# Optimization experiments

Hardware: AMD Instinct MI355X
Metric: run time of the kernel (lower is better)

Reference implementation:

```python
import jax, jax.numpy as jnp
import numpy as np

B, T, D, E, H = 4, 2048, 1024, 8, 1024  # H = hidden_units // num_experts


def setup_inputs() -> dict:
    key = jax.random.key(0)
    ks = jax.random.split(key, 5)
    s = 0.02
    return {
        "x": jax.random.normal(ks[0], (B, T, D), dtype=jnp.float32),
        "Wp": jax.random.normal(ks[1], (D, E), dtype=jnp.float32) * s,
        "bp": jnp.zeros((E,), dtype=jnp.float32),
        "W1": jax.random.normal(ks[2], (E, D, H), dtype=jnp.float32) * s,
        "b1": jnp.zeros((E, H), dtype=jnp.float32),
        "W2": jax.random.normal(ks[3], (E, H, D), dtype=jnp.float32) * s,
        "b2": jnp.zeros((E, D), dtype=jnp.float32),
    }


def reference(x, Wp, bp, W1, b1, W2, b2):
    b, t, d = x.shape
    e = Wp.shape[1]
    xf = x.reshape(-1, d)                       # [N, D]
    logits = xf @ Wp + bp                       # [N, E]
    probs = jax.nn.softmax(logits, axis=-1)     # [N, E]
    expert_chosen = jnp.argmax(probs, axis=-1)  # top-1 routing, [N]
    expert_probs = jnp.take_along_axis(probs, expert_chosen[:, None], axis=-1)  # [N,1]

    # Dense masked dispatch/combine (same math as gather-FFN-scatter; ReLU FFN,
    # dropout_rate=0 so dropout is identity).
    out = jnp.zeros_like(xf)
    for i in range(e):
        h = jax.nn.relu(xf @ W1[i] + b1[i])     # [N, H]
        y = h @ W2[i] + b2[i]                   # [N, D]
        mask = (expert_chosen == i).astype(xf.dtype)[:, None]
        out = out + mask * y

    # probs / probs.detach() == 1 in forward; gradient-routing trick preserved.
    out = out * (expert_probs / jax.lax.stop_gradient(expert_probs))
    return out.reshape(b, t, d), probs.reshape(b, t, e), expert_chosen.reshape(b, t)
```

## Files before the change

### kernel.cpp

```cpp
#include <hip/hip_runtime.h>
#include <stdint.h>

#define N_TOK 8192
#define D_DIM 1024
#define E_NUM 8

typedef float f32x4 __attribute__((ext_vector_type(4)));
typedef __bf16 bf16x8 __attribute__((ext_vector_type(8)));

__device__ __forceinline__ unsigned short f32_to_bf16_bits(float f) {
  union { float f; uint32_t u; } v; v.f = f;
  uint32_t u = v.u;
  uint32_t r = u + 0x7fffu + ((u >> 16) & 1u);
  return (unsigned short)(r >> 16);
}

__device__ __forceinline__ void load_lds16(const void* g, void* l) {
  __builtin_amdgcn_global_load_lds(
      (const __attribute__((address_space(1))) void*)g,
      (__attribute__((address_space(3))) void*)l, 16, 0, 0);
}

__device__ __forceinline__ void transpose_tile(unsigned short (*T)[72],
                                               const float* __restrict__ S,
                                               unsigned short* __restrict__ O,
                                               int r0, int c0, int t) {
  const int rr = t >> 4;
  const int cc = (t & 15) * 4;
#pragma unroll
  for (int p = 0; p < 4; p++) {
    int r = p * 16 + rr;
    float4 v = *reinterpret_cast<const float4*>(S + (size_t)(r0 + r) * 1024 + c0 + cc);
    T[cc + 0][r] = f32_to_bf16_bits(v.x);
    T[cc + 1][r] = f32_to_bf16_bits(v.y);
    T[cc + 2][r] = f32_to_bf16_bits(v.z);
    T[cc + 3][r] = f32_to_bf16_bits(v.w);
  }
  __syncthreads();
#pragma unroll
  for (int p = 0; p < 4; p++) {
    int c = p * 16 + rr;
    ushort4 o = *reinterpret_cast<const ushort4*>(&T[c][cc]);
    *reinterpret_cast<ushort4*>(O + (size_t)(c0 + c) * 1024 + r0 + cc) = o;
  }
}

__global__ __launch_bounds__(256) void wpt_kernel(const float* __restrict__ Wp,
                                                  float* __restrict__ WpT) {
  int i = blockIdx.x * 256 + threadIdx.x;
  int e = i >> 10, d = i & 1023;
  WpT[i] = Wp[(size_t)d * E_NUM + e];
}

__global__ __launch_bounds__(256) void routing_w1t_kernel(
    const float* __restrict__ x, const float* __restrict__ WpT,
    const float* __restrict__ bp, float* __restrict__ probs_out,
    float* __restrict__ chosenF, int* __restrict__ chosen,
    unsigned short* __restrict__ xb,
    const float* __restrict__ W1, unsigned short* __restrict__ W1t) {
  __shared__ __align__(16) unsigned short T[64][72];
  __shared__ __align__(16) float pbuf[4][8];
  if (blockIdx.x >= 2048) {
    const int tb = blockIdx.x - 2048;
    const int e = tb >> 8, rc = tb & 255;
    transpose_tile(T, W1 + ((size_t)e << 20), W1t + ((size_t)e << 20),
                   (rc >> 4) * 64, (rc & 15) * 64, threadIdx.x);
    return;
  }
  const int wave = threadIdx.x >> 6;
  const int lane = threadIdx.x & 63;
  const int token = blockIdx.x * 4 + wave;
  const float* xr = x + (size_t)token * D_DIM;
  unsigned short* xbr = xb + (size_t)token * D_DIM;
  double acc[E_NUM];
#pragma unroll
  for (int e = 0; e < E_NUM; e++) acc[e] = 0.0;
#pragma unroll
  for (int it = 0; it < 4; it++) {
    const int d0 = it * 256 + lane * 4;
    float4 xv = *reinterpret_cast<const float4*>(xr + d0);
    ushort4 o;
    o.x = f32_to_bf16_bits(xv.x);
    o.y = f32_to_bf16_bits(xv.y);
    o.z = f32_to_bf16_bits(xv.z);
    o.w = f32_to_bf16_bits(xv.w);
    *reinterpret_cast<ushort4*>(xbr + d0) = o;
#pragma unroll
    for (int e = 0; e < E_NUM; e++) {
      float4 w = *reinterpret_cast<const float4*>(WpT + (e << 10) + d0);
      acc[e] += (double)xv.x * (double)w.x;
      acc[e] += (double)xv.y * (double)w.y;
      acc[e] += (double)xv.z * (double)w.z;
      acc[e] += (double)xv.w * (double)w.w;
    }
  }
#pragma unroll
  for (int e = 0; e < E_NUM; e++) {
#pragma unroll
    for (int off = 32; off > 0; off >>= 1) acc[e] += __shfl_xor(acc[e], off);
  }
  if (lane == 0) {
    double lg[E_NUM];
#pragma unroll
    for (int e = 0; e < E_NUM; e++) lg[e] = acc[e] + (double)bp[e];
    int best = 0;
    double bv = lg[0];
#pragma unroll
    for (int e = 1; e < E_NUM; e++)
      if (lg[e] > bv) { bv = lg[e]; best = e; }
    double s = 0.0, ex[E_NUM];
#pragma unroll
    for (int e = 0; e < E_NUM; e++) { ex[e] = exp(lg[e] - bv); s += ex[e]; }
    double inv = 1.0 / s;
#pragma unroll
    for (int e = 0; e < E_NUM; e++) pbuf[wave][e] = (float)(ex[e] * inv);
    chosenF[token] = (float)best;
    chosen[token] = best;
  }
  __syncthreads();
  if (threadIdx.x < 8) {
    float4 v = *reinterpret_cast<const float4*>(
        &pbuf[threadIdx.x >> 1][(threadIdx.x & 1) * 4]);
    reinterpret_cast<float4*>(probs_out + (size_t)blockIdx.x * 32)[threadIdx.x] = v;
  }
}

__global__ __launch_bounds__(256) void scan_scatter_kernel(
    const int* __restrict__ chosen, int* __restrict__ offsets,
    int* __restrict__ perm) {
  __shared__ int hist[E_NUM];
  __shared__ int cur;
  const int e = blockIdx.x;
  const int t = threadIdx.x;
  if (t < E_NUM) hist[t] = 0;
  __syncthreads();
  for (int n = t; n < N_TOK; n += 256) atomicAdd(&hist[chosen[n]], 1);
  __syncthreads();
  if (t == 0) {
    int off = 0;
    for (int i = 0; i < e; i++) off += hist[i];
    cur = off;
    if (e == 0) {
      int o = 0;
      for (int i = 0; i < E_NUM; i++) { offsets[i] = o; o += hist[i]; }
      offsets[E_NUM] = o;
    }
  }
  __syncthreads();
  for (int n = t; n < N_TOK; n += 256) {
    if (chosen[n] == e) {
      int p = atomicAdd(&cur, 1);
      perm[p] = n;
    }
  }
}

__global__ __launch_bounds__(256) void transpose_cast_kernel(
    const float* __restrict__ src, unsigned short* __restrict__ dst) {
  __shared__ __align__(16) unsigned short T[64][72];
  const int e = blockIdx.z;
  transpose_tile(T, src + ((size_t)e << 20), dst + ((size_t)e << 20),
                 blockIdx.y * 64, blockIdx.x * 64, threadIdx.x);
}

template <int MODE, int BK>
__global__ __launch_bounds__(256) void moe_gemm_kernel(
    const unsigned short* __restrict__ Abase,
    const unsigned short* __restrict__ Wt,
    const float* __restrict__ bias,
    const int* __restrict__ offsets, const int* __restrict__ perm,
    unsigned short* __restrict__ hb, float* __restrict__ out,
    const float* __restrict__ tsrc, unsigned short* __restrict__ tdst,
    int gemm_blocks) {
  constexpr int NCH = BK / 8;
  constexpr int RPL = 64 / NCH;
  constexpr int ALW = 32 / RPL;
  constexpr int BLW = 16 / RPL;
  constexpr int KSTEPS = 1024 / BK;
  __shared__ __align__(16) unsigned short As[2][128 * BK];
  __shared__ __align__(16) unsigned short Bs[2][64 * BK];

  if ((int)blockIdx.x >= gemm_blocks) {
    const int tb = blockIdx.x - gemm_blocks;
    const int e = tb >> 8, rc = tb & 255;
    auto T = reinterpret_cast<unsigned short(*)[72]>(&As[0][0]);
    transpose_tile(T, tsrc + ((size_t)e << 20), tdst + ((size_t)e << 20),
                   (rc >> 4) * 64, (rc & 15) * 64, threadIdx.x);
    return;
  }

  const int e = blockIdx.x & 7;
  const int slot = blockIdx.x >> 3;
  const int g0 = offsets[e];
  const int m_count = offsets[e + 1] - g0;
  const int m0 = (slot >> 4) * 128;
  if (m0 >= m_count) return;
  const int n0 = (slot & 15) * 64;

  const int tid = threadIdx.x;
  const int wid = tid >> 6, lane = tid & 63;
  const int lrow = lane / NCH;
  const int lchunk = lane & (NCH - 1);
  const int schunk = lchunk ^ (lrow & (NCH - 1));

  const unsigned short* ga[ALW];
  const unsigned short* gb[BLW];
  int abase[ALW], bbase[BLW];
  const unsigned short* WtE = Wt + ((size_t)e << 20);
#pragma unroll
  for (int t = 0; t < ALW; t++) {
    const int rbase = (wid * ALW + t) * RPL;
    const int r = rbase + lrow;
    int gr = g0 + m0 + r;
    if (gr > N_TOK - 1) gr = N_TOK - 1;
    const int arow = (MODE == 0) ? perm[gr] : gr;
    ga[t] = Abase + (size_t)arow * 1024 + schunk * 8;
    abase[t] = rbase * BK;
  }
#pragma unroll
  for (int t = 0; t < BLW; t++) {
    const int rbase = (wid * BLW + t) * RPL;
    const int r = rbase + lrow;
    gb[t] = WtE + (size_t)(n0 + r) * 1024 + schunk * 8;
    bbase[t] = rbase * BK;
  }

  f32x4 acc[4][2];
  const f32x4 zero4 = {0.f, 0.f, 0.f, 0.f};
#pragma unroll
  for (int i = 0; i < 4; i++)
#pragma unroll
    for (int j = 0; j < 2; j++) acc[i][j] = zero4;

  const int wr = wid >> 1, wc = wid & 1;
  const int lr = lane & 15, lk = lane >> 4;

  auto stage = [&](int buf) {
#pragma unroll
    for (int t = 0; t < ALW; t++) {
      load_lds16(ga[t], &As[buf][abase[t]]);
      ga[t] += BK;
    }
#pragma unroll
    for (int t = 0; t < BLW; t++) {
      load_lds16(gb[t], &Bs[buf][bbase[t]]);
      gb[t] += BK;
    }
  };
  auto compute = [&](int buf) {
#pragma unroll
    for (int kk = 0; kk < BK; kk += 32) {
      bf16x8 af[4], bfr[2];
#pragma unroll
      for (int mf = 0; mf < 4; mf++) {
        const int ra = wr * 64 + mf * 16 + lr;
        const int ca = ((kk >> 3) + lk) ^ (ra & (NCH - 1));
        af[mf] = *reinterpret_cast<const bf16x8*>(&As[buf][ra * BK + ca * 8]);
      }
#pragma unroll
      for (int nf = 0; nf < 2; nf++) {
        const int rb = wc * 32 + nf * 16 + lr;
        const int cb = ((kk >> 3) + lk) ^ (rb & (NCH - 1));
        bfr[nf] = *reinterpret_cast<const bf16x8*>(&Bs[buf][rb * BK + cb * 8]);
      }
#pragma unroll
      for (int mf = 0; mf < 4; mf++)
#pragma unroll
        for (int nf = 0; nf < 2; nf++)
          acc[mf][nf] = __builtin_amdgcn_mfma_f32_16x16x32_bf16(
              af[mf], bfr[nf], acc[mf][nf], 0, 0, 0);
    }
  };

  stage(0);
  stage(1);
#pragma unroll
  for (int kt = 0; kt < KSTEPS; kt++) {
    if (kt < KSTEPS - 1) {
      if constexpr (BK == 64)
        asm volatile("s_waitcnt vmcnt(6)" ::: "memory");
      else
        asm volatile("s_waitcnt vmcnt(3)" ::: "memory");
    } else {
      asm volatile("s_waitcnt vmcnt(0)" ::: "memory");
    }
    __builtin_amdgcn_sched_barrier(0);
    __builtin_amdgcn_s_barrier();
    __builtin_amdgcn_s_setprio(1);
    compute(kt & 1);
    __builtin_amdgcn_s_setprio(0);
    __builtin_amdgcn_s_barrier();
    if (kt < KSTEPS - 2) stage(kt & 1);
  }

  const int mlim = m_count - m0;
#pragma unroll
  for (int nf = 0; nf < 2; nf++) {
    const int c = n0 + wc * 32 + nf * 16 + lr;
    const float bval = bias[(e << 10) + c];
#pragma unroll
    for (int mf = 0; mf < 4; mf++) {
#pragma unroll
      for (int j = 0; j < 4; j++) {
        const int lrow2 = wr * 64 + mf * 16 + lk * 4 + j;
        if (lrow2 < mlim) {
          float v = acc[mf][nf][j] + bval;
          if (MODE == 0) {
            v = v > 0.f ? v : 0.f;
            hb[(size_t)(g0 + m0 + lrow2) * 1024 + c] = f32_to_bf16_bits(v);
          } else {
            int token = perm[g0 + m0 + lrow2];
            out[(size_t)token * 1024 + c] = v;
          }
        }
      }
    }
  }
}

extern "C" void kernel_launch(void* const* d_in, const int* in_sizes, int n_in,
                              void* d_out, int out_size, void* d_ws, size_t ws_size,
                              hipStream_t stream) {
  const float* x = (const float*)d_in[0];
  const float* Wp = (const float*)d_in[1];
  const float* bp = (const float*)d_in[2];
  const float* W1 = (const float*)d_in[3];
  const float* b1 = (const float*)d_in[4];
  const float* W2 = (const float*)d_in[5];
  const float* b2 = (const float*)d_in[6];

  float* out = (float*)d_out;
  float* probs = out + (size_t)N_TOK * D_DIM;
  float* chosenF = probs + (size_t)N_TOK * E_NUM;

  char* ws = (char*)d_ws;
  int* chosen = (int*)(ws + 0);
  int* perm = (int*)(ws + 32768);
  float* WpT = (float*)(ws + 65536);
  int* offsets = (int*)(ws + 98304);
  const size_t MB16 = 16777216;
  unsigned short* xb = (unsigned short*)(ws + 131072);
  unsigned short* Wt1 = (unsigned short*)(ws + 131072 + MB16);
  const bool overlap = ws_size >= 131072 + 4 * MB16;
  unsigned short* Wt2 = (unsigned short*)(ws + 131072 + (overlap ? 2 : 1) * MB16);
  unsigned short* hb = (unsigned short*)(ws + 131072 + (overlap ? 3 : 2) * MB16);

  const int GEMM_BLOCKS = E_NUM * 64 * 16;

  wpt_kernel<<<32, 256, 0, stream>>>(Wp, WpT);
  routing_w1t_kernel<<<4096, 256, 0, stream>>>(x, WpT, bp, probs, chosenF, chosen,
                                               xb, W1, Wt1);
  scan_scatter_kernel<<<E_NUM, 256, 0, stream>>>(chosen, offsets, perm);
  if (overlap) {
    moe_gemm_kernel<0, 32><<<GEMM_BLOCKS + 2048, 256, 0, stream>>>(
        xb, Wt1, b1, offsets, perm, hb, nullptr, W2, Wt2, GEMM_BLOCKS);
  } else {
    moe_gemm_kernel<0, 32><<<GEMM_BLOCKS, 256, 0, stream>>>(
        xb, Wt1, b1, offsets, perm, hb, nullptr, nullptr, nullptr, GEMM_BLOCKS);
    transpose_cast_kernel<<<dim3(16, 16, 8), 256, 0, stream>>>(W2, Wt2);
  }
  moe_gemm_kernel<1, 64><<<GEMM_BLOCKS, 256, 0, stream>>>(
      hb, Wt2, b2, offsets, perm, nullptr, out, nullptr, nullptr, GEMM_BLOCKS);
}
```

Before: 130.5 us.

## Use 256x128 triple-buffered GEMM for first MoE layer; move W2 transpose earlier

Adds a new first-layer expert GEMM kernel with 512 threads, 256x128 output tiles and a three-stage LDS ring. The next stage is issued right after the barrier, which removes the second barrier per k-step and raises operand reuse per block. The W2 transpose/cast blocks move out of the GEMM1 launch and into the routing kernel's grid, so GEMM1 runs only GEMM work. In exchange, about 144KB of LDS limits each CU to one block, and the larger tiles add padding waste for experts whose token count is not a multiple of 256.

```diff
diff --git a/kernel.cpp b/kernel.cpp
--- a/kernel.cpp
+++ b/kernel.cpp
@@ -57,9 +57,17 @@
     const float* __restrict__ bp, float* __restrict__ probs_out,
     float* __restrict__ chosenF, int* __restrict__ chosen,
     unsigned short* __restrict__ xb,
-    const float* __restrict__ W1, unsigned short* __restrict__ W1t) {
+    const float* __restrict__ W1, unsigned short* __restrict__ W1t,
+    const float* __restrict__ W2, unsigned short* __restrict__ W2t) {
   __shared__ __align__(16) unsigned short T[64][72];
   __shared__ __align__(16) float pbuf[4][8];
+  if (blockIdx.x >= 4096) {
+    const int tb = blockIdx.x - 4096;
+    const int e = tb >> 8, rc = tb & 255;
+    transpose_tile(T, W2 + ((size_t)e << 20), W2t + ((size_t)e << 20),
+                   (rc >> 4) * 64, (rc & 15) * 64, threadIdx.x);
+    return;
+  }
   if (blockIdx.x >= 2048) {
     const int tb = blockIdx.x - 2048;
     const int e = tb >> 8, rc = tb & 255;
@@ -163,110 +171,94 @@
                  blockIdx.y * 64, blockIdx.x * 64, threadIdx.x);
 }
 
-template <int MODE, int BK>
-__global__ __launch_bounds__(256) void moe_gemm_kernel(
+template <int MODE>
+__global__ __launch_bounds__(512, 1) void moe_gemm_deep_kernel(
     const unsigned short* __restrict__ Abase,
     const unsigned short* __restrict__ Wt,
     const float* __restrict__ bias,
     const int* __restrict__ offsets, const int* __restrict__ perm,
-    unsigned short* __restrict__ hb, float* __restrict__ out,
-    const float* __restrict__ tsrc, unsigned short* __restrict__ tdst,
-    int gemm_blocks) {
-  constexpr int NCH = BK / 8;
-  constexpr int RPL = 64 / NCH;
-  constexpr int ALW = 32 / RPL;
-  constexpr int BLW = 16 / RPL;
-  constexpr int KSTEPS = 1024 / BK;
-  __shared__ __align__(16) unsigned short As[2][128 * BK];
-  __shared__ __align__(16) unsigned short Bs[2][64 * BK];
-
-  if ((int)blockIdx.x >= gemm_blocks) {
-    const int tb = blockIdx.x - gemm_blocks;
-    const int e = tb >> 8, rc = tb & 255;
-    auto T = reinterpret_cast<unsigned short(*)[72]>(&As[0][0]);
-    transpose_tile(T, tsrc + ((size_t)e << 20), tdst + ((size_t)e << 20),
-                   (rc >> 4) * 64, (rc & 15) * 64, threadIdx.x);
-    return;
-  }
+    unsigned short* __restrict__ hb, float* __restrict__ out) {
+  __shared__ __align__(16) unsigned short As[3][256 * 64];
+  __shared__ __align__(16) unsigned short Bs[3][128 * 64];
 
   const int e = blockIdx.x & 7;
   const int slot = blockIdx.x >> 3;
   const int g0 = offsets[e];
   const int m_count = offsets[e + 1] - g0;
-  const int m0 = (slot >> 4) * 128;
+  const int m0 = (slot >> 3) * 256;
   if (m0 >= m_count) return;
-  const int n0 = (slot & 15) * 64;
+  const int n0 = (slot & 7) * 128;
 
   const int tid = threadIdx.x;
   const int wid = tid >> 6, lane = tid & 63;
-  const int lrow = lane / NCH;
-  const int lchunk = lane & (NCH - 1);
-  const int schunk = lchunk ^ (lrow & (NCH - 1));
-
-  const unsigned short* ga[ALW];
-  const unsigned short* gb[BLW];
-  int abase[ALW], bbase[BLW];
+  const int lrow = lane >> 3;
+  const int lchunk = lane & 7;
+  const int schunk = lchunk ^ lrow;
+
+  const unsigned short* ga[4];
+  const unsigned short* gb[2];
+  int abase[4], bbase[2];
   const unsigned short* WtE = Wt + ((size_t)e << 20);
 #pragma unroll
-  for (int t = 0; t < ALW; t++) {
-    const int rbase = (wid * ALW + t) * RPL;
+  for (int t = 0; t < 4; t++) {
+    const int rbase = (wid * 4 + t) * 8;
     const int r = rbase + lrow;
     int gr = g0 + m0 + r;
     if (gr > N_TOK - 1) gr = N_TOK - 1;
     const int arow = (MODE == 0) ? perm[gr] : gr;
     ga[t] = Abase + (size_t)arow * 1024 + schunk * 8;
-    abase[t] = rbase * BK;
-  }
-#pragma unroll
-  for (int t = 0; t < BLW; t++) {
-    const int rbase = (wid * BLW + t) * RPL;
+    abase[t] = rbase * 64;
+  }
+#pragma unroll
+  for (int t = 0; t < 2; t++) {
+    const int rbase = (wid * 2 + t) * 8;
     const int r = rbase + lrow;
     gb[t] = WtE + (size_t)(n0 + r) * 1024 + schunk * 8;
-    bbase[t] = rbase * BK;
-  }
-
-  f32x4 acc[4][2];
+    bbase[t] = rbase * 64;
+  }
+
+  f32x4 acc[4][4];
   const f32x4 zero4 = {0.f, 0.f, 0.f, 0.f};
 #pragma unroll
   for (int i = 0; i < 4; i++)
 #pragma unroll
-    for (int j = 0; j < 2; j++) acc[i][j] = zero4;
+    for (int j = 0; j < 4; j++) acc[i][j] = zero4;
 
   const int wr = wid >> 1, wc = wid & 1;
   const int lr = lane & 15, lk = lane >> 4;
 
   auto stage = [&](int buf) {
 #pragma unroll
-    for (int t = 0; t < ALW; t++) {
+    for (int t = 0; t < 4; t++) {
       load_lds16(ga[t], &As[buf][abase[t]]);
-      ga[t] += BK;
-    }
-#pragma unroll
-    for (int t = 0; t < BLW; t++) {
+      ga[t] += 64;
+    }
+#pragma unroll
+    for (int t = 0; t < 2; t++) {
       load_lds16(gb[t], &Bs[buf][bbase[t]]);
-      gb[t] += BK;
+      gb[t] += 64;
     }
   };
   auto compute = [&](int buf) {
 #pragma unroll
-    for (int kk = 0; kk < BK; kk += 32) {
-      bf16x8 af[4], bfr[2];
+    for (int kk = 0; kk < 64; kk += 32) {
+      bf16x8 af[4], bfr[4];
 #pragma unroll
       for (int mf = 0; mf < 4; mf++) {
         const int ra = wr * 64 + mf * 16 + lr;
-        const int ca = ((kk >> 3) + lk) ^ (ra & (NCH - 1));
-        af[mf] = *reinterpret_cast<const bf16x8*>(&As[buf][ra * BK + ca * 8]);
-      }
-#pragma unroll
-      for (int nf = 0; nf < 2; nf++) {
-        const int rb = wc * 32 + nf * 16 + lr;
-        const int cb = ((kk >> 3) + lk) ^ (rb & (NCH - 1));
-        bfr[nf] = *reinterpret_cast<const bf16x8*>(&Bs[buf][rb * BK + cb * 8]);
+        const int ca = ((kk >> 3) + lk) ^ (ra & 7);
+        af[mf] = *reinterpret_cast<const bf16x8*>(&As[buf][ra * 64 + ca * 8]);
+      }
+#pragma unroll
+      for (int nf = 0; nf < 4; nf++) {
+        const int rb = wc * 64 + nf * 16 + lr;
+        const int cb = ((kk >> 3) + lk) ^ (rb & 7);
+        bfr[nf] = *reinterpret_cast<const bf16x8*>(&Bs[buf][rb * 64 + cb * 8]);
       }
 #pragma unroll
       for (int mf = 0; mf < 4; mf++)
 #pragma unroll
-        for (int nf = 0; nf < 2; nf++)
+        for (int nf = 0; nf < 4; nf++)
           acc[mf][nf] = __builtin_amdgcn_mfma_f32_16x16x32_bf16(
               af[mf], bfr[nf], acc[mf][nf], 0, 0, 0);
     }
@@ -275,28 +267,24 @@
   stage(0);
   stage(1);
 #pragma unroll
-  for (int kt = 0; kt < KSTEPS; kt++) {
-    if (kt < KSTEPS - 1) {
-      if constexpr (BK == 64)
-        asm volatile("s_waitcnt vmcnt(6)" ::: "memory");
-      else
-        asm volatile("s_waitcnt vmcnt(3)" ::: "memory");
+  for (int kt = 0; kt < 16; kt++) {
+    if (kt < 15) {
+      asm volatile("s_waitcnt vmcnt(6)" ::: "memory");
     } else {
       asm volatile("s_waitcnt vmcnt(0)" ::: "memory");
     }
     __builtin_amdgcn_sched_barrier(0);
     __builtin_amdgcn_s_barrier();
+    if (kt < 14) stage((kt + 2) % 3);
     __builtin_amdgcn_s_setprio(1);
-    compute(kt & 1);
+    compute(kt % 3);
     __builtin_amdgcn_s_setprio(0);
-    __builtin_amdgcn_s_barrier();
-    if (kt < KSTEPS - 2) stage(kt & 1);
   }
 
   const int mlim = m_count - m0;
 #pragma unroll
-  for (int nf = 0; nf < 2; nf++) {
-    const int c = n0 + wc * 32 + nf * 16 + lr;
+  for (int nf = 0; nf < 4; nf++) {
+    const int c = n0 + wc * 64 + nf * 16 + lr;
     const float bval = bias[(e << 10) + c];
 #pragma unroll
     for (int mf = 0; mf < 4; mf++) {
@@ -318,6 +306,148 @@
   }
 }
 
+template <int MODE, int BK>
+__global__ __launch_bounds__(256) void moe_gemm_kernel(
+    const unsigned short* __restrict__ Abase,
+    const unsigned short* __restrict__ Wt,
+    const float* __restrict__ bias,
+    const int* __restrict__ offsets, const int* __restrict__ perm,
+    unsigned short* __restrict__ hb, float* __restrict__ out,
+    int gemm_blocks) {
+  constexpr int NCH = BK / 8;
+  constexpr int RPL = 64 / NCH;
+  constexpr int ALW = 32 / RPL;
+  constexpr int BLW = 16 / RPL;
+  constexpr int KSTEPS = 1024 / BK;
+  __shared__ __align__(16) unsigned short As[2][128 * BK];
+  __shared__ __align__(16) unsigned short Bs[2][64 * BK];
+
+  const int e = blockIdx.x & 7;
+  const int slot = blockIdx.x >> 3;
+  const int g0 = offsets[e];
+  const int m_count = offsets[e + 1] - g0;
+  const int m0 = (slot >> 4) * 128;
+  if (m0 >= m_count) return;
+  const int n0 = (slot & 15) * 64;
+
+  const int tid = threadIdx.x;
+  const int wid = tid >> 6, lane = tid & 63;
+  const int lrow = lane / NCH;
+  const int lchunk = lane & (NCH - 1);
+  const int schunk = lchunk ^ (lrow & (NCH - 1));
+
+  const unsigned short* ga[ALW];
+  const unsigned short* gb[BLW];
+  int abase[ALW], bbase[BLW];
+  const unsigned short* WtE = Wt + ((size_t)e << 20);
+#pragma unroll
+  for (int t = 0; t < ALW; t++) {
+    const int rbase = (wid * ALW + t) * RPL;
+    const int r = rbase + lrow;
+    int gr = g0 + m0 + r;
+    if (gr > N_TOK - 1) gr = N_TOK - 1;
+    const int arow = (MODE == 0) ? perm[gr] : gr;
+    ga[t] = Abase + (size_t)arow * 1024 + schunk * 8;
+    abase[t] = rbase * BK;
+  }
+#pragma unroll
+  for (int t = 0; t < BLW; t++) {
+    const int rbase = (wid * BLW + t) * RPL;
+    const int r = rbase + lrow;
+    gb[t] = WtE + (size_t)(n0 + r) * 1024 + schunk * 8;
+    bbase[t] = rbase * BK;
+  }
+
+  f32x4 acc[4][2];
+  const f32x4 zero4 = {0.f, 0.f, 0.f, 0.f};
+#pragma unroll
+  for (int i = 0; i < 4; i++)
+#pragma unroll
+    for (int j = 0; j < 2; j++) acc[i][j] = zero4;
+
+  const int wr = wid >> 1, wc = wid & 1;
+  const int lr = lane & 15, lk = lane >> 4;
+
+  auto stage = [&](int buf) {
+#pragma unroll
+    for (int t = 0; t < ALW; t++) {
+      load_lds16(ga[t], &As[buf][abase[t]]);
+      ga[t] += BK;
+    }
+#pragma unroll
+    for (int t = 0; t < BLW; t++) {
+      load_lds16(gb[t], &Bs[buf][bbase[t]]);
+      gb[t] += BK;
+    }
+  };
+  auto compute = [&](int buf) {
+#pragma unroll
+    for (int kk = 0; kk < BK; kk += 32) {
+      bf16x8 af[4], bfr[2];
+#pragma unroll
+      for (int mf = 0; mf < 4; mf++) {
+        const int ra = wr * 64 + mf * 16 + lr;
+        const int ca = ((kk >> 3) + lk) ^ (ra & (NCH - 1));
+        af[mf] = *reinterpret_cast<const bf16x8*>(&As[buf][ra * BK + ca * 8]);
+      }
+#pragma unroll
+      for (int nf = 0; nf < 2; nf++) {
+        const int rb = wc * 32 + nf * 16 + lr;
+        const int cb = ((kk >> 3) + lk) ^ (rb & (NCH - 1));
+        bfr[nf] = *reinterpret_cast<const bf16x8*>(&Bs[buf][rb * BK + cb * 8]);
+      }
+#pragma unroll
+      for (int mf = 0; mf < 4; mf++)
+#pragma unroll
+        for (int nf = 0; nf < 2; nf++)
+          acc[mf][nf] = __builtin_amdgcn_mfma_f32_16x16x32_bf16(
+              af[mf], bfr[nf], acc[mf][nf], 0, 0, 0);
+    }
+  };
+
+  stage(0);
+  stage(1);
+#pragma unroll
+  for (int kt = 0; kt < KSTEPS; kt++) {
+    if (kt < KSTEPS - 1) {
+      asm volatile("s_waitcnt vmcnt(6)" ::: "memory");
+    } else {
+      asm volatile("s_waitcnt vmcnt(0)" ::: "memory");
+    }
+    __builtin_amdgcn_sched_barrier(0);
+    __builtin_amdgcn_s_barrier();
+    __builtin_amdgcn_s_setprio(1);
+    compute(kt & 1);
+    __builtin_amdgcn_s_setprio(0);
+    __builtin_amdgcn_s_barrier();
+    if (kt < KSTEPS - 2) stage(kt & 1);
+  }
+
+  const int mlim = m_count - m0;
+#pragma unroll
+  for (int nf = 0; nf < 2; nf++) {
+    const int c = n0 + wc * 32 + nf * 16 + lr;
+    const float bval = bias[(e << 10) + c];
+#pragma unroll
+    for (int mf = 0; mf < 4; mf++) {
+#pragma unroll
+      for (int j = 0; j < 4; j++) {
+        const int lrow2 = wr * 64 + mf * 16 + lk * 4 + j;
+        if (lrow2 < mlim) {
+          float v = acc[mf][nf][j] + bval;
+          if (MODE == 0) {
+            v = v > 0.f ? v : 0.f;
+            hb[(size_t)(g0 + m0 + lrow2) * 1024 + c] = f32_to_bf16_bits(v);
+          } else {
+            int token = perm[g0 + m0 + lrow2];
+            out[(size_t)token * 1024 + c] = v;
+          }
+        }
+      }
+    }
+  }
+}
+
 extern "C" void kernel_launch(void* const* d_in, const int* in_sizes, int n_in,
                               void* d_out, int out_size, void* d_ws, size_t ws_size,
                               hipStream_t stream) {
@@ -345,20 +475,15 @@
   unsigned short* Wt2 = (unsigned short*)(ws + 131072 + (overlap ? 2 : 1) * MB16);
   unsigned short* hb = (unsigned short*)(ws + 131072 + (overlap ? 3 : 2) * MB16);
 
-  const int GEMM_BLOCKS = E_NUM * 64 * 16;
-
   wpt_kernel<<<32, 256, 0, stream>>>(Wp, WpT);
-  routing_w1t_kernel<<<4096, 256, 0, stream>>>(x, WpT, bp, probs, chosenF, chosen,
-                                               xb, W1, Wt1);
+  routing_w1t_kernel<<<overlap ? 6144 : 4096, 256, 0, stream>>>(
+      x, WpT, bp, probs, chosenF, chosen, xb, W1, Wt1, W2, Wt2);
   scan_scatter_kernel<<<E_NUM, 256, 0, stream>>>(chosen, offsets, perm);
-  if (overlap) {
-    moe_gemm_kernel<0, 32><<<GEMM_BLOCKS + 2048, 256, 0, stream>>>(
-        xb, Wt1, b1, offsets, perm, hb, nullptr, W2, Wt2, GEMM_BLOCKS);
-  } else {
-    moe_gemm_kernel<0, 32><<<GEMM_BLOCKS, 256, 0, stream>>>(
-        xb, Wt1, b1, offsets, perm, hb, nullptr, nullptr, nullptr, GEMM_BLOCKS);
+  moe_gemm_deep_kernel<0><<<E_NUM * 32 * 8, 512, 0, stream>>>(
+      xb, Wt1, b1, offsets, perm, hb, nullptr);
+  if (!overlap) {
     transpose_cast_kernel<<<dim3(16, 16, 8), 256, 0, stream>>>(W2, Wt2);
   }
-  moe_gemm_kernel<1, 64><<<GEMM_BLOCKS, 256, 0, stream>>>(
-      hb, Wt2, b2, offsets, perm, nullptr, out, nullptr, nullptr, GEMM_BLOCKS);
-}
+  moe_gemm_kernel<1, 64><<<E_NUM * 64 * 16, 256, 0, stream>>>(
+      hb, Wt2, b2, offsets, perm, nullptr, out, E_NUM * 64 * 16);
+}
```

After: 149.5 us. 14.6% more time.
